# Optimization experiments

Measured on AMD Instinct MI355X. Metric: run time of the kernel, lower is better.

The kernel has to match this reference:

```python
import jax, jax.numpy as jnp
import numpy as np

NEG_SLOPE = 0.2  # PyG GATConv default negative_slope


def _segment_softmax(alpha, dst, n):
    m = jax.ops.segment_max(alpha, dst, num_segments=n)
    m = jnp.where(jnp.isfinite(m), m, 0.0)
    ex = jnp.exp(alpha - m[dst])
    den = jax.ops.segment_sum(ex, dst, num_segments=n)
    return ex / (den[dst] + 1e-16)


def _gat_layer(x, src, dst, eattr, W, att_src, att_dst, We, att_e, b, n):
    h = x @ W                                        # [N, C]
    a = (h @ att_src)[src] + (h @ att_dst)[dst] + (eattr @ We) @ att_e  # [E]
    a = jax.nn.leaky_relu(a, NEG_SLOPE)
    coef = _segment_softmax(a, dst, n)               # edge-wise attention
    out = jax.ops.segment_sum(coef[:, None] * h[src], dst, num_segments=n)
    return out + b


def _glorot(key, shape):
    fan_in, fan_out = shape[0], shape[-1]
    s = jnp.sqrt(6.0 / (fan_in + fan_out))
    return jax.random.uniform(key, shape, jnp.float32, -s, s)


def setup_inputs() -> dict:
    N, E, D, ED = 100000, 1600000, 128, 16
    key = jax.random.key(0)
    ks = jax.random.split(key, 32)
    inp = {
        'x': jax.random.normal(ks[0], (N, D), jnp.float32),
        'edge_index': jax.random.randint(ks[1], (2, E), 0, N, jnp.int64),
        'edge_attr': jax.random.normal(ks[2], (E, ED), jnp.float32),
    }
    dims = [(D, 64), (64, 32), (32, 16)]
    i = 3
    for li, (din, dout) in enumerate(dims, 1):
        inp[f'W{li}'] = _glorot(ks[i], (din, dout)); i += 1
        inp[f'att_src{li}'] = _glorot(ks[i], (dout,)); i += 1
        inp[f'att_dst{li}'] = _glorot(ks[i], (dout,)); i += 1
        inp[f'We{li}'] = _glorot(ks[i], (ED, dout)); i += 1
        inp[f'att_e{li}'] = _glorot(ks[i], (dout,)); i += 1
        inp[f'b{li}'] = jnp.zeros((dout,), jnp.float32)
    return inp


def reference(x, edge_index, edge_attr,
              W1, att_src1, att_dst1, We1, att_e1, b1,
              W2, att_src2, att_dst2, We2, att_e2, b2,
              W3, att_src3, att_dst3, We3, att_e3, b3):
    n = x.shape[0]
    src, dst = edge_index[0], edge_index[1]
    # add self-loops; self-loop edge_attr = mean of incoming edge attrs (fill_value='mean')
    cnt = jax.ops.segment_sum(jnp.ones_like(dst, dtype=edge_attr.dtype), dst, num_segments=n)
    loop_attr = jax.ops.segment_sum(edge_attr, dst, num_segments=n) / jnp.maximum(cnt, 1.0)[:, None]
    loops = jnp.arange(n, dtype=src.dtype)
    src2 = jnp.concatenate([src, loops])
    dst2 = jnp.concatenate([dst, loops])
    ea2 = jnp.concatenate([edge_attr, loop_attr], axis=0)

    h = jax.nn.elu(_gat_layer(x, src2, dst2, ea2, W1, att_src1, att_dst1, We1, att_e1, b1, n))
    h = jax.nn.elu(_gat_layer(h, src2, dst2, ea2, W2, att_src2, att_dst2, We2, att_e2, b2, n))
    z = _gat_layer(h, src2, dst2, ea2, W3, att_src3, att_dst3, We3, att_e3, b3, n)
    return z
```

## Files before the change

### kernel.cpp

```cpp
#include <hip/hip_runtime.h>
#include <hip/hip_bf16.h>

typedef __hip_bfloat16 bf16;

__device__ __forceinline__ float lrelu(float a) { return a > 0.f ? a : 0.2f * a; }
__device__ __forceinline__ int clampi(int v, int hi) { return v < 0 ? 0 : (v >= hi ? hi - 1 : v); }
__device__ __forceinline__ float ldx(const void* p, size_t i, int f32) {
  return f32 ? ((const float*)p)[i] : (float)((const bf16*)p)[i];
}
__device__ __forceinline__ float4 ldx4(const void* p, size_t i, int f32) {
  if (f32) return *(const float4*)((const float*)p + i);
  const __hip_bfloat162* q = (const __hip_bfloat162*)((const bf16*)p + i);
  float2 a = __bfloat1622float2(q[0]), b = __bfloat1622float2(q[1]);
  return make_float4(a.x, a.y, b.x, b.y);
}

__global__ __launch_bounds__(256) void detect_k(const int* __restrict__ ei32,
                                                const unsigned short* __restrict__ xw, int E,
                                                int* __restrict__ flags) {
  __shared__ int s64, sf;
  int t = threadIdx.x;
  if (t == 0) { s64 = 1; sf = 0; }
  __syncthreads();
  int lim = E < 2048 ? E : 2048;
  for (int k = t; k < lim; k += 256)
    if (ei32[2 * k + 1] != 0) atomicAnd(&s64, 0);
  int hit = 0;
  for (int k = t; k < 4096; k += 256) {
    int ex = (xw[k] >> 7) & 0xFF;
    if (ex >= 0xC3) hit = 1;
  }
  if (hit) atomicOr(&sf, 1);
  __syncthreads();
  if (t == 0) { flags[0] = s64; flags[1] = sf; }
}

__global__ __launch_bounds__(256) void count_k(const int* __restrict__ ei32, int E, int N,
                                               const int* __restrict__ flags,
                                               int* __restrict__ cnt) {
  int e = blockIdx.x * blockDim.x + threadIdx.x;
  if (e >= E) return;
  int is64 = flags[0] != 0;
  int d = is64 ? ei32[2 * ((size_t)E + e)] : ei32[(size_t)E + e];
  atomicAdd(&cnt[clampi(d, N)], 1);
}

__global__ __launch_bounds__(1024) void scan1_k(const int* __restrict__ cnt, int* __restrict__ excl,
                                                int* __restrict__ bsum, int n) {
  __shared__ int sh[1024];
  int i = blockIdx.x * 1024 + threadIdx.x;
  int v = (i < n) ? cnt[i] : 0;
  sh[threadIdx.x] = v;
  __syncthreads();
  for (int off = 1; off < 1024; off <<= 1) {
    int t = (threadIdx.x >= off) ? sh[threadIdx.x - off] : 0;
    __syncthreads();
    sh[threadIdx.x] += t;
    __syncthreads();
  }
  if (i < n) excl[i] = sh[threadIdx.x] - v;
  if (threadIdx.x == 1023) bsum[blockIdx.x] = sh[1023];
}

__global__ __launch_bounds__(128) void scan2_k(int* bsum, int nb) {
  __shared__ int sh[128];
  int t = threadIdx.x;
  int v = (t < nb) ? bsum[t] : 0;
  sh[t] = v;
  __syncthreads();
  for (int off = 1; off < 128; off <<= 1) {
    int x = (t >= off) ? sh[t - off] : 0;
    __syncthreads();
    sh[t] += x;
    __syncthreads();
  }
  if (t < nb) bsum[t] = sh[t] - v;
}

__global__ __launch_bounds__(256) void scan3_k(int* __restrict__ row_ptr,
                                               const int* __restrict__ bsum,
                                               int* __restrict__ cur, int n, int E) {
  int i = blockIdx.x * blockDim.x + threadIdx.x;
  if (i < n) {
    int r = row_ptr[i] + bsum[i >> 10];
    row_ptr[i] = r;
    cur[i] = r;
  }
  if (i == 0) row_ptr[n] = E;
}

__global__ __launch_bounds__(64) void wvec_k(const void* We1, const void* ae1, const void* We2,
                                             const void* ae2, const void* We3, const void* ae3,
                                             const int* __restrict__ flags, float* wv) {
  int t = threadIdx.x;
  if (t >= 48) return;
  int f32 = flags[1];
  int l = t >> 4, j = t & 15;
  const void* We = l == 0 ? We1 : (l == 1 ? We2 : We3);
  const void* ae = l == 0 ? ae1 : (l == 1 ? ae2 : ae3);
  int C = l == 0 ? 64 : (l == 1 ? 32 : 16);
  float s = 0.f;
  for (int c = 0; c < C; ++c) s += ldx(We, (size_t)j * C + c, f32) * ldx(ae, c, f32);
  wv[l * 16 + j] = s;
}

__global__ __launch_bounds__(256) void scatter_k(const int* __restrict__ ei32, const void* eattr,
                                                 const float* __restrict__ wv,
                                                 const int* __restrict__ flags,
                                                 int* __restrict__ cur,
                                                 float4* __restrict__ recs, int E, int N) {
  __shared__ float w[48];
  if (threadIdx.x < 48) w[threadIdx.x] = wv[threadIdx.x];
  __syncthreads();
  int e = blockIdx.x * 256 + threadIdx.x;
  if (e >= E) return;
  int is64 = flags[0] != 0, f32 = flags[1] != 0;
  int s = is64 ? ei32[2 * (size_t)e] : ei32[e];
  int d = is64 ? ei32[2 * ((size_t)E + e)] : ei32[(size_t)E + e];
  s = clampi(s, N);
  d = clampi(d, N);
  float v[16];
  if (f32) {
    const float4* p = (const float4*)((const float*)eattr + (size_t)e * 16);
#pragma unroll
    for (int j = 0; j < 4; ++j) {
      float4 t = p[j];
      v[4 * j] = t.x; v[4 * j + 1] = t.y; v[4 * j + 2] = t.z; v[4 * j + 3] = t.w;
    }
  } else {
    const __hip_bfloat162* p = (const __hip_bfloat162*)((const bf16*)eattr + (size_t)e * 16);
#pragma unroll
    for (int j = 0; j < 8; ++j) {
      float2 t = __bfloat1622float2(p[j]);
      v[2 * j] = t.x; v[2 * j + 1] = t.y;
    }
  }
  float q1 = 0.f, q2 = 0.f, q3 = 0.f;
#pragma unroll
  for (int j = 0; j < 16; ++j) {
    q1 += v[j] * w[j];
    q2 += v[j] * w[16 + j];
    q3 += v[j] * w[32 + j];
  }
  int pos = clampi(atomicAdd(&cur[d], 1), E);
  recs[pos] = make_float4(__int_as_float(s), q1, q2, q3);
}

template <int K, int C, bool XEXT>
__global__ __launch_bounds__(256, 4) void mm3_k(const void* Xv, const void* Wv, const void* ats_v,
                                                const void* atd_v, const int* __restrict__ flags,
                                                int N, float* __restrict__ h,
                                                float* __restrict__ as_, float* __restrict__ ad_) {
  static_assert(K == 2 * C, "");
  constexpr int NCG = C / 8;
  constexpr int TM = 512 / NCG;
  __shared__ __align__(16) float Wl[K * C];
  __shared__ __align__(16) float Xl[32 * TM];
  const int f32 = flags[1];
  const int tid = threadIdx.x;
  for (int i = tid; i < K * C; i += 256) Wl[i] = ldx(Wv, i, f32);
  const int cg = tid & (NCG - 1);
  const int ng = tid / NCG;
  const int c0 = cg * 8;
  float ats[8], atd[8];
#pragma unroll
  for (int j = 0; j < 8; ++j) {
    ats[j] = ldx(ats_v, c0 + j, f32);
    atd[j] = ldx(atd_v, c0 + j, f32);
  }
  const int n_base = blockIdx.x * TM;
  float acc[2][8];
#pragma unroll
  for (int i = 0; i < 2; ++i)
#pragma unroll
    for (int j = 0; j < 8; ++j) acc[i][j] = 0.f;

#pragma unroll 1
  for (int kc = 0; kc < K / 32; ++kc) {
    __syncthreads();
#pragma unroll
    for (int t = 0; t < TM / 32; ++t) {
      int f = tid + t * 256;
      int node = f >> 3, kq = f & 7;
      int gn = n_base + node;
      if (gn >= N) gn = N - 1;
      float4 v;
      if (XEXT)
        v = ldx4(Xv, (size_t)gn * K + kc * 32 + kq * 4, f32);
      else
        v = *(const float4*)((const float*)Xv + (size_t)gn * K + kc * 32 + kq * 4);
      int col = node ^ (kq * 4);
      Xl[(kq * 4 + 0) * TM + col] = v.x;
      Xl[(kq * 4 + 1) * TM + col] = v.y;
      Xl[(kq * 4 + 2) * TM + col] = v.z;
      Xl[(kq * 4 + 3) * TM + col] = v.w;
    }
    __syncthreads();
#pragma unroll 8
    for (int kk = 0; kk < 32; ++kk) {
      const float2 xv = *(const float2*)&Xl[kk * TM + ((2 * ng) ^ ((kk >> 2) * 4))];
      const float4 w0 = *(const float4*)&Wl[(kc * 32 + kk) * C + c0];
      const float4 w1 = *(const float4*)&Wl[(kc * 32 + kk) * C + c0 + 4];
      const float ws[8] = {w0.x, w0.y, w0.z, w0.w, w1.x, w1.y, w1.z, w1.w};
#pragma unroll
      for (int j = 0; j < 8; ++j) {
        acc[0][j] += xv.x * ws[j];
        acc[1][j] += xv.y * ws[j];
      }
    }
  }
#pragma unroll
  for (int i = 0; i < 2; ++i) {
    int n = n_base + ng * 2 + i;
    float vs = 0.f, vd = 0.f;
#pragma unroll
    for (int j = 0; j < 8; ++j) {
      vs += acc[i][j] * ats[j];
      vd += acc[i][j] * atd[j];
    }
#pragma unroll
    for (int off = NCG / 2; off > 0; off >>= 1) {
      vs += __shfl_xor(vs, off, NCG);
      vd += __shfl_xor(vd, off, NCG);
    }
    if (n < N) {
      float* hr = &h[(size_t)n * C + c0];
      *(float4*)hr = make_float4(acc[i][0], acc[i][1], acc[i][2], acc[i][3]);
      *(float4*)(hr + 4) = make_float4(acc[i][4], acc[i][5], acc[i][6], acc[i][7]);
      if (cg == 0) {
        as_[n] = vs;
        ad_[n] = vd;
      }
    }
  }
}

template <int C, int QC, bool ELU, bool LAST>
__global__ __launch_bounds__(256) void agg_k(const int* __restrict__ row_ptr,
                                             const float4* __restrict__ recs,
                                             const float* __restrict__ as_,
                                             const float* __restrict__ ad_,
                                             const float* __restrict__ h, const void* b,
                                             const int* __restrict__ flags, void* out, int N,
                                             int E) {
  const int GR = 256 / C;
  __shared__ int ss[256];
  __shared__ float sp[256];
  int lane = threadIdx.x & (C - 1);
  int grp = threadIdx.x / C;
  int slot0 = grp * C;
  int f32 = flags[1];
  float bc = ldx(b, lane, f32);
  for (int n = blockIdx.x * GR + grp; n < N; n += gridDim.x * GR) {
    int start = row_ptr[n], end = row_ptr[n + 1];
    int deg = end > start ? end - start : 0;
    float qsum = 0.f;
    for (int j = lane; j < deg; j += C) {
      float4 r = recs[start + j];
      qsum += ((const float*)&r)[QC];
    }
#pragma unroll
    for (int off = C / 2; off > 0; off >>= 1) qsum += __shfl_xor(qsum, off, C);
    float qloop = qsum / fmaxf((float)deg, 1.0f);
    float adn = ad_[n];
    float m = lrelu(as_[n] + adn + qloop), den = 1.0f;
    float acc = h[(size_t)n * C + lane];
    for (int base = 0; base < deg; base += C) {
      int cnt = deg - base < C ? deg - base : C;
      int sj = 0;
      float aj = -1e30f;
      if (lane < cnt) {
        float4 r = recs[start + base + lane];
        sj = clampi(__float_as_int(r.x), N);
        aj = lrelu(as_[sj] + adn + ((const float*)&r)[QC]);
      }
      float cm = aj;
#pragma unroll
      for (int off = C / 2; off > 0; off >>= 1) cm = fmaxf(cm, __shfl_xor(cm, off, C));
      float nm = fmaxf(m, cm);
      float sc = __expf(m - nm);
      float pj = (lane < cnt) ? __expf(aj - nm) : 0.f;
      float ps = pj;
#pragma unroll
      for (int off = C / 2; off > 0; off >>= 1) ps += __shfl_xor(ps, off, C);
      den = den * sc + ps;
      m = nm;
      ss[slot0 + lane] = sj;
      sp[slot0 + lane] = pj;
      float accs = 0.f;
#pragma unroll 8
      for (int jj = 0; jj < cnt; ++jj) {
        int s = ss[slot0 + jj];
        float p = sp[slot0 + jj];
        accs += p * h[(size_t)s * C + lane];
      }
      acc = acc * sc + accs;
    }
    float o = acc / (den + 1e-16f) + bc;
    if (ELU) o = o > 0.f ? o : (__expf(o) - 1.0f);
    if (LAST && !f32)
      ((bf16*)out)[(size_t)n * C + lane] = (bf16)o;
    else
      ((float*)out)[(size_t)n * C + lane] = o;
  }
}

extern "C" void kernel_launch(void* const* d_in, const int* in_sizes, int n_in, void* d_out,
                              int out_size, void* d_ws, size_t ws_size, hipStream_t stream) {
  const void* x = d_in[0];
  const int* ei32 = (const int*)d_in[1];
  void* eattr = d_in[2];
  const void *W1 = d_in[3], *s1 = d_in[4], *t1 = d_in[5], *We1 = d_in[6], *ae1 = d_in[7],
             *b1 = d_in[8];
  const void *W2 = d_in[9], *s2 = d_in[10], *t2 = d_in[11], *We2 = d_in[12], *ae2 = d_in[13],
             *b2 = d_in[14];
  const void *W3 = d_in[15], *s3 = d_in[16], *t3 = d_in[17], *We3 = d_in[18], *ae3 = d_in[19],
             *b3 = d_in[20];

  const int N = in_sizes[0] / 128;
  const int E = in_sizes[1] / 2;

  char* p = (char*)d_ws;
  auto alloc = [&](size_t bytes) -> void* {
    void* r = (void*)p;
    p += (bytes + 255) & ~(size_t)255;
    return r;
  };
  int* row_ptr = (int*)alloc((size_t)(N + 1) * 4);
  float4* recs = (float4*)alloc((size_t)E * 16);
  int* cnt = (int*)alloc((size_t)N * 4);
  int* cur = (int*)alloc((size_t)N * 4);
  int* bsum = (int*)alloc(128 * 4);
  float* wv = (float*)alloc(64 * 4);
  int* flags = (int*)alloc(256);
  float* as_ = (float*)alloc((size_t)N * 4);
  float* ad_ = (float*)alloc((size_t)N * 4);
  size_t used = (size_t)(p - (char*)d_ws);
  size_t need = 2 * ((size_t)N * 64 * 4 + 256);
  float *bufH, *bufO;
  if (used + need <= ws_size) {
    bufH = (float*)alloc((size_t)N * 64 * 4);
    bufO = (float*)alloc((size_t)N * 64 * 4);
  } else {
    bufH = (float*)eattr;
    bufO = (float*)eattr + (size_t)N * 64;
  }

  hipMemsetAsync(cnt, 0, (size_t)N * 4, stream);
  detect_k<<<1, 256, 0, stream>>>(ei32, (const unsigned short*)x, E, flags);
  count_k<<<(E + 255) / 256, 256, 0, stream>>>(ei32, E, N, flags, cnt);
  int nb = (N + 1023) / 1024;
  scan1_k<<<nb, 1024, 0, stream>>>(cnt, row_ptr, bsum, N);
  scan2_k<<<1, 128, 0, stream>>>(bsum, nb);
  scan3_k<<<(N + 255) / 256, 256, 0, stream>>>(row_ptr, bsum, cur, N, E);
  wvec_k<<<1, 64, 0, stream>>>(We1, ae1, We2, ae2, We3, ae3, flags, wv);
  scatter_k<<<(E + 255) / 256, 256, 0, stream>>>(ei32, eattr, wv, flags, cur, recs, E, N);

  mm3_k<128, 64, true><<<(N + 63) / 64, 256, 0, stream>>>(x, W1, s1, t1, flags, N, bufH, as_, ad_);
  agg_k<64, 1, true, false><<<(N + 3) / 4, 256, 0, stream>>>(row_ptr, recs, as_, ad_, bufH, b1,
                                                             flags, bufO, N, E);
  mm3_k<64, 32, false><<<(N + 127) / 128, 256, 0, stream>>>(bufO, W2, s2, t2, flags, N, bufH, as_,
                                                            ad_);
  agg_k<32, 2, true, false><<<(N + 7) / 8, 256, 0, stream>>>(row_ptr, recs, as_, ad_, bufH, b2,
                                                             flags, bufO, N, E);
  mm3_k<32, 16, false><<<(N + 255) / 256, 256, 0, stream>>>(bufO, W3, s3, t3, flags, N, bufH, as_,
                                                            ad_);
  agg_k<16, 3, false, true><<<(N + 15) / 16, 256, 0, stream>>>(row_ptr, recs, as_, ad_, bufH, b3,
                                                               flags, d_out, N, E);
}
```

Baseline: 588.6 us.

## Replace global atomic CSR scatter with two-pass bucketed binning and local sort

Edges are binned into 32-node buckets in a staging buffer (reusing the hidden-feature buffers), with the in-degree count fused into the same pass, so the separate count kernel goes away. A per-bucket sort kernel then places records into CSR order using shared-memory atomics and writes contiguously. This aims to cut the scattered global atomics and random 16-byte writes of the old scatter, in exchange for an extra staging write and read and an overflow path for buckets that exceed capacity. Per-bucket counters are padded 64 bytes apart to avoid contention.

```diff
diff --git a/kernel.cpp b/kernel.cpp
--- a/kernel.cpp
+++ b/kernel.cpp
@@ -13,6 +13,33 @@
   const __hip_bfloat162* q = (const __hip_bfloat162*)((const bf16*)p + i);
   float2 a = __bfloat1622float2(q[0]), b = __bfloat1622float2(q[1]);
   return make_float4(a.x, a.y, b.x, b.y);
+}
+
+__device__ __forceinline__ void edge_qs(const void* eattr, size_t e, int f32, const float* w,
+                                        float& q1, float& q2, float& q3) {
+  float v[16];
+  if (f32) {
+    const float4* p = (const float4*)((const float*)eattr + e * 16);
+#pragma unroll
+    for (int j = 0; j < 4; ++j) {
+      float4 t = p[j];
+      v[4 * j] = t.x; v[4 * j + 1] = t.y; v[4 * j + 2] = t.z; v[4 * j + 3] = t.w;
+    }
+  } else {
+    const __hip_bfloat162* p = (const __hip_bfloat162*)((const bf16*)eattr + e * 16);
+#pragma unroll
+    for (int j = 0; j < 8; ++j) {
+      float2 t = __bfloat1622float2(p[j]);
+      v[2 * j] = t.x; v[2 * j + 1] = t.y;
+    }
+  }
+  q1 = 0.f; q2 = 0.f; q3 = 0.f;
+#pragma unroll
+  for (int j = 0; j < 16; ++j) {
+    q1 += v[j] * w[j];
+    q2 += v[j] * w[16 + j];
+    q3 += v[j] * w[32 + j];
+  }
 }
 
 __global__ __launch_bounds__(256) void detect_k(const int* __restrict__ ei32,
@@ -104,6 +131,81 @@
   wv[l * 16 + j] = s;
 }
 
+__global__ __launch_bounds__(256) void bin_k(const int* __restrict__ ei32, const void* eattr,
+                                             const float* __restrict__ wv,
+                                             const int* __restrict__ flags, int* __restrict__ cnt,
+                                             int* __restrict__ bcnt, float4* __restrict__ stage,
+                                             int* __restrict__ ovf, int* __restrict__ ovfc, int E,
+                                             int N, int CAP) {
+  __shared__ float w[48];
+  if (threadIdx.x < 48) w[threadIdx.x] = wv[threadIdx.x];
+  __syncthreads();
+  int e = blockIdx.x * 256 + threadIdx.x;
+  if (e >= E) return;
+  int is64 = flags[0] != 0, f32 = flags[1] != 0;
+  int s = is64 ? ei32[2 * (size_t)e] : ei32[e];
+  int d = is64 ? ei32[2 * ((size_t)E + e)] : ei32[(size_t)E + e];
+  s = clampi(s, N);
+  d = clampi(d, N);
+  atomicAdd(&cnt[d], 1);
+  float q1, q2, q3;
+  edge_qs(eattr, (size_t)e, f32, w, q1, q2, q3);
+  int b = d >> 5;
+  int lpos = atomicAdd(&bcnt[b * 16], 1);
+  if (lpos < CAP) {
+    unsigned u = (unsigned)s | ((unsigned)(d & 31) << 20);
+    stage[(size_t)b * CAP + lpos] = make_float4(__uint_as_float(u), q1, q2, q3);
+  } else {
+    int oi = atomicAdd(ovfc, 1);
+    if (oi < E) ovf[oi] = e;
+  }
+}
+
+__global__ __launch_bounds__(256) void sort_k(const int* __restrict__ row_ptr,
+                                              const int* __restrict__ bcnt,
+                                              const float4* __restrict__ stage,
+                                              const int* __restrict__ ovf,
+                                              const int* __restrict__ ovfc,
+                                              const int* __restrict__ ei32, const void* eattr,
+                                              const float* __restrict__ wv,
+                                              const int* __restrict__ flags,
+                                              float4* __restrict__ recs, int E, int N, int CAP) {
+  __shared__ int hcur[32];
+  int b = blockIdx.x;
+  int tid = threadIdx.x;
+  if (tid < 32) hcur[tid] = 0;
+  __syncthreads();
+  int node0 = b << 5;
+  int nrec = bcnt[b * 16];
+  if (nrec > CAP) nrec = CAP;
+  for (int i = tid; i < nrec; i += 256) {
+    float4 r = stage[(size_t)b * CAP + i];
+    unsigned u = __float_as_uint(r.x);
+    int s = (int)(u & 0xFFFFFu);
+    int drel = (int)(u >> 20);
+    int pos = row_ptr[node0 + drel] + atomicAdd(&hcur[drel], 1);
+    recs[clampi(pos, E)] = make_float4(__int_as_float(s), r.y, r.z, r.w);
+  }
+  int oc = *ovfc;
+  if (oc > 0) {
+    if (oc > E) oc = E;
+    __syncthreads();
+    int is64 = flags[0] != 0, f32 = flags[1] != 0;
+    for (int i = tid; i < oc; i += 256) {
+      int e = ovf[i];
+      int d = is64 ? ei32[2 * ((size_t)E + e)] : ei32[(size_t)E + e];
+      d = clampi(d, N);
+      if ((d >> 5) != b) continue;
+      int s = is64 ? ei32[2 * (size_t)e] : ei32[e];
+      s = clampi(s, N);
+      float q1, q2, q3;
+      edge_qs(eattr, (size_t)e, f32, wv, q1, q2, q3);
+      int pos = row_ptr[d] + atomicAdd(&hcur[d & 31], 1);
+      recs[clampi(pos, E)] = make_float4(__int_as_float(s), q1, q2, q3);
+    }
+  }
+}
+
 __global__ __launch_bounds__(256) void scatter_k(const int* __restrict__ ei32, const void* eattr,
                                                  const float* __restrict__ wv,
                                                  const int* __restrict__ flags,
@@ -119,29 +221,8 @@
   int d = is64 ? ei32[2 * ((size_t)E + e)] : ei32[(size_t)E + e];
   s = clampi(s, N);
   d = clampi(d, N);
-  float v[16];
-  if (f32) {
-    const float4* p = (const float4*)((const float*)eattr + (size_t)e * 16);
-#pragma unroll
-    for (int j = 0; j < 4; ++j) {
-      float4 t = p[j];
-      v[4 * j] = t.x; v[4 * j + 1] = t.y; v[4 * j + 2] = t.z; v[4 * j + 3] = t.w;
-    }
-  } else {
-    const __hip_bfloat162* p = (const __hip_bfloat162*)((const bf16*)eattr + (size_t)e * 16);
-#pragma unroll
-    for (int j = 0; j < 8; ++j) {
-      float2 t = __bfloat1622float2(p[j]);
-      v[2 * j] = t.x; v[2 * j + 1] = t.y;
-    }
-  }
-  float q1 = 0.f, q2 = 0.f, q3 = 0.f;
-#pragma unroll
-  for (int j = 0; j < 16; ++j) {
-    q1 += v[j] * w[j];
-    q2 += v[j] * w[16 + j];
-    q3 += v[j] * w[32 + j];
-  }
+  float q1, q2, q3;
+  edge_qs(eattr, (size_t)e, f32, w, q1, q2, q3);
   int pos = clampi(atomicAdd(&cur[d], 1), E);
   recs[pos] = make_float4(__int_as_float(s), q1, q2, q3);
 }
@@ -319,6 +400,7 @@
 
   const int N = in_sizes[0] / 128;
   const int E = in_sizes[1] / 2;
+  const int B = (N + 31) >> 5;
 
   char* p = (char*)d_ws;
   auto alloc = [&](size_t bytes) -> void* {
@@ -335,26 +417,45 @@
   int* flags = (int*)alloc(256);
   float* as_ = (float*)alloc((size_t)N * 4);
   float* ad_ = (float*)alloc((size_t)N * 4);
+  int* bcnt = (int*)alloc((size_t)B * 16 * 4);
+  int* ovf = (int*)alloc((size_t)E * 4);
+  int* ovfc = (int*)alloc(256);
   size_t used = (size_t)(p - (char*)d_ws);
   size_t need = 2 * ((size_t)N * 64 * 4 + 256);
   float *bufH, *bufO;
-  if (used + need <= ws_size) {
+  bool hasbuf = used + need <= ws_size;
+  if (hasbuf) {
     bufH = (float*)alloc((size_t)N * 64 * 4);
     bufO = (float*)alloc((size_t)N * 64 * 4);
   } else {
     bufH = (float*)eattr;
     bufO = (float*)eattr + (size_t)N * 64;
   }
+  size_t stage_bytes = 2 * ((size_t)N * 64 * 4);
+  int CAP = (int)(stage_bytes / ((size_t)B * 16));
+  bool binned = hasbuf && N <= (1 << 20) && CAP >= 64;
 
   hipMemsetAsync(cnt, 0, (size_t)N * 4, stream);
   detect_k<<<1, 256, 0, stream>>>(ei32, (const unsigned short*)x, E, flags);
-  count_k<<<(E + 255) / 256, 256, 0, stream>>>(ei32, E, N, flags, cnt);
+  wvec_k<<<1, 64, 0, stream>>>(We1, ae1, We2, ae2, We3, ae3, flags, wv);
   int nb = (N + 1023) / 1024;
-  scan1_k<<<nb, 1024, 0, stream>>>(cnt, row_ptr, bsum, N);
-  scan2_k<<<1, 128, 0, stream>>>(bsum, nb);
-  scan3_k<<<(N + 255) / 256, 256, 0, stream>>>(row_ptr, bsum, cur, N, E);
-  wvec_k<<<1, 64, 0, stream>>>(We1, ae1, We2, ae2, We3, ae3, flags, wv);
-  scatter_k<<<(E + 255) / 256, 256, 0, stream>>>(ei32, eattr, wv, flags, cur, recs, E, N);
+  if (binned) {
+    hipMemsetAsync(bcnt, 0, (size_t)B * 16 * 4, stream);
+    hipMemsetAsync(ovfc, 0, 4, stream);
+    bin_k<<<(E + 255) / 256, 256, 0, stream>>>(ei32, eattr, wv, flags, cnt, bcnt, (float4*)bufH,
+                                               ovf, ovfc, E, N, CAP);
+    scan1_k<<<nb, 1024, 0, stream>>>(cnt, row_ptr, bsum, N);
+    scan2_k<<<1, 128, 0, stream>>>(bsum, nb);
+    scan3_k<<<(N + 255) / 256, 256, 0, stream>>>(row_ptr, bsum, cur, N, E);
+    sort_k<<<B, 256, 0, stream>>>(row_ptr, bcnt, (const float4*)bufH, ovf, ovfc, ei32, eattr, wv,
+                                  flags, recs, E, N, CAP);
+  } else {
+    count_k<<<(E + 255) / 256, 256, 0, stream>>>(ei32, E, N, flags, cnt);
+    scan1_k<<<nb, 1024, 0, stream>>>(cnt, row_ptr, bsum, N);
+    scan2_k<<<1, 128, 0, stream>>>(bsum, nb);
+    scan3_k<<<(N + 255) / 256, 256, 0, stream>>>(row_ptr, bsum, cur, N, E);
+    scatter_k<<<(E + 255) / 256, 256, 0, stream>>>(ei32, eattr, wv, flags, cur, recs, E, N);
+  }
 
   mm3_k<128, 64, true><<<(N + 63) / 64, 256, 0, stream>>>(x, W1, s1, t1, flags, N, bufH, as_, ad_);
   agg_k<64, 1, true, false><<<(N + 3) / 4, 256, 0, stream>>>(row_ptr, recs, as_, ad_, bufH, b1,
```

After: 598.3 us. No clear change (+1.7%).

## Fuse edge scatter into first-layer matmul launch and fold scan passes

Applied to the files above, without the earlier changes.

Merges the edge-record scatter kernel with the first-layer matmul into one launch, where extra blocks beyond the matmul grid handle 1024 edges each with four edges per thread. It also folds the block-sum scan into scan3 when there are at most 128 blocks, and makes count_k process four edges per thread. The intent is to cut launch overhead and let the memory-bound scatter run alongside the compute-heavy matmul. The fused kernel carries the matmul's shared-memory footprint into the scatter blocks, and every scan3 block redundantly rescans the block sums.

```diff
diff --git a/kernel.cpp b/kernel.cpp
--- a/kernel.cpp
+++ b/kernel.cpp
@@ -13,6 +13,33 @@
   const __hip_bfloat162* q = (const __hip_bfloat162*)((const bf16*)p + i);
   float2 a = __bfloat1622float2(q[0]), b = __bfloat1622float2(q[1]);
   return make_float4(a.x, a.y, b.x, b.y);
+}
+
+__device__ __forceinline__ void edge_qs(const void* eattr, size_t e, int f32, const float* w,
+                                        float& q1, float& q2, float& q3) {
+  float v[16];
+  if (f32) {
+    const float4* p = (const float4*)((const float*)eattr + e * 16);
+#pragma unroll
+    for (int j = 0; j < 4; ++j) {
+      float4 t = p[j];
+      v[4 * j] = t.x; v[4 * j + 1] = t.y; v[4 * j + 2] = t.z; v[4 * j + 3] = t.w;
+    }
+  } else {
+    const __hip_bfloat162* p = (const __hip_bfloat162*)((const bf16*)eattr + e * 16);
+#pragma unroll
+    for (int j = 0; j < 8; ++j) {
+      float2 t = __bfloat1622float2(p[j]);
+      v[2 * j] = t.x; v[2 * j + 1] = t.y;
+    }
+  }
+  q1 = 0.f; q2 = 0.f; q3 = 0.f;
+#pragma unroll
+  for (int j = 0; j < 16; ++j) {
+    q1 += v[j] * w[j];
+    q2 += v[j] * w[16 + j];
+    q3 += v[j] * w[32 + j];
+  }
 }
 
 __global__ __launch_bounds__(256) void detect_k(const int* __restrict__ ei32,
@@ -38,11 +65,16 @@
 __global__ __launch_bounds__(256) void count_k(const int* __restrict__ ei32, int E, int N,
                                                const int* __restrict__ flags,
                                                int* __restrict__ cnt) {
-  int e = blockIdx.x * blockDim.x + threadIdx.x;
-  if (e >= E) return;
   int is64 = flags[0] != 0;
-  int d = is64 ? ei32[2 * ((size_t)E + e)] : ei32[(size_t)E + e];
-  atomicAdd(&cnt[clampi(d, N)], 1);
+  int e0 = blockIdx.x * 1024 + threadIdx.x;
+#pragma unroll
+  for (int i = 0; i < 4; ++i) {
+    int e = e0 + i * 256;
+    if (e < E) {
+      int d = is64 ? ei32[2 * ((size_t)E + e)] : ei32[(size_t)E + e];
+      atomicAdd(&cnt[clampi(d, N)], 1);
+    }
+  }
 }
 
 __global__ __launch_bounds__(1024) void scan1_k(const int* __restrict__ cnt, int* __restrict__ excl,
@@ -77,12 +109,28 @@
   if (t < nb) bsum[t] = sh[t] - v;
 }
 
+template <bool FOLD>
 __global__ __launch_bounds__(256) void scan3_k(int* __restrict__ row_ptr,
                                                const int* __restrict__ bsum,
-                                               int* __restrict__ cur, int n, int E) {
-  int i = blockIdx.x * blockDim.x + threadIdx.x;
+                                               int* __restrict__ cur, int n, int E, int nb) {
+  __shared__ int pref[128];
+  int t = threadIdx.x;
+  if (FOLD) {
+    if (t < 128) pref[t] = (t < nb) ? bsum[t] : 0;
+    __syncthreads();
+    for (int off = 1; off < 128; off <<= 1) {
+      int x = 0;
+      if (t < 128 && t >= off) x = pref[t - off];
+      __syncthreads();
+      if (t < 128) pref[t] += x;
+      __syncthreads();
+    }
+  }
+  int i = blockIdx.x * 256 + t;
   if (i < n) {
-    int r = row_ptr[i] + bsum[i >> 10];
+    int blk = i >> 10;
+    int add = FOLD ? (blk == 0 ? 0 : pref[blk - 1]) : bsum[blk];
+    int r = row_ptr[i] + add;
     row_ptr[i] = r;
     cur[i] = r;
   }
@@ -104,59 +152,14 @@
   wv[l * 16 + j] = s;
 }
 
-__global__ __launch_bounds__(256) void scatter_k(const int* __restrict__ ei32, const void* eattr,
-                                                 const float* __restrict__ wv,
-                                                 const int* __restrict__ flags,
-                                                 int* __restrict__ cur,
-                                                 float4* __restrict__ recs, int E, int N) {
-  __shared__ float w[48];
-  if (threadIdx.x < 48) w[threadIdx.x] = wv[threadIdx.x];
-  __syncthreads();
-  int e = blockIdx.x * 256 + threadIdx.x;
-  if (e >= E) return;
-  int is64 = flags[0] != 0, f32 = flags[1] != 0;
-  int s = is64 ? ei32[2 * (size_t)e] : ei32[e];
-  int d = is64 ? ei32[2 * ((size_t)E + e)] : ei32[(size_t)E + e];
-  s = clampi(s, N);
-  d = clampi(d, N);
-  float v[16];
-  if (f32) {
-    const float4* p = (const float4*)((const float*)eattr + (size_t)e * 16);
-#pragma unroll
-    for (int j = 0; j < 4; ++j) {
-      float4 t = p[j];
-      v[4 * j] = t.x; v[4 * j + 1] = t.y; v[4 * j + 2] = t.z; v[4 * j + 3] = t.w;
-    }
-  } else {
-    const __hip_bfloat162* p = (const __hip_bfloat162*)((const bf16*)eattr + (size_t)e * 16);
-#pragma unroll
-    for (int j = 0; j < 8; ++j) {
-      float2 t = __bfloat1622float2(p[j]);
-      v[2 * j] = t.x; v[2 * j + 1] = t.y;
-    }
-  }
-  float q1 = 0.f, q2 = 0.f, q3 = 0.f;
-#pragma unroll
-  for (int j = 0; j < 16; ++j) {
-    q1 += v[j] * w[j];
-    q2 += v[j] * w[16 + j];
-    q3 += v[j] * w[32 + j];
-  }
-  int pos = clampi(atomicAdd(&cur[d], 1), E);
-  recs[pos] = make_float4(__int_as_float(s), q1, q2, q3);
-}
-
 template <int K, int C, bool XEXT>
-__global__ __launch_bounds__(256, 4) void mm3_k(const void* Xv, const void* Wv, const void* ats_v,
-                                                const void* atd_v, const int* __restrict__ flags,
-                                                int N, float* __restrict__ h,
-                                                float* __restrict__ as_, float* __restrict__ ad_) {
+__device__ __forceinline__ void mm_body(const void* Xv, const void* Wv, const void* ats_v,
+                                        const void* atd_v, int f32, int N, int nblk, float* Wl,
+                                        float* Xl, float* __restrict__ h, float* __restrict__ as_,
+                                        float* __restrict__ ad_) {
   static_assert(K == 2 * C, "");
   constexpr int NCG = C / 8;
   constexpr int TM = 512 / NCG;
-  __shared__ __align__(16) float Wl[K * C];
-  __shared__ __align__(16) float Xl[32 * TM];
-  const int f32 = flags[1];
   const int tid = threadIdx.x;
   for (int i = tid; i < K * C; i += 256) Wl[i] = ldx(Wv, i, f32);
   const int cg = tid & (NCG - 1);
@@ -168,7 +171,7 @@
     ats[j] = ldx(ats_v, c0 + j, f32);
     atd[j] = ldx(atd_v, c0 + j, f32);
   }
-  const int n_base = blockIdx.x * TM;
+  const int n_base = nblk * TM;
   float acc[2][8];
 #pragma unroll
   for (int i = 0; i < 2; ++i)
@@ -233,6 +236,66 @@
       }
     }
   }
+}
+
+template <int K, int C, bool XEXT>
+__global__ __launch_bounds__(256, 4) void mm3_k(const void* Xv, const void* Wv, const void* ats_v,
+                                                const void* atd_v, const int* __restrict__ flags,
+                                                int N, float* __restrict__ h,
+                                                float* __restrict__ as_, float* __restrict__ ad_) {
+  constexpr int TM = 512 / (C / 8);
+  __shared__ __align__(16) float Wl[K * C];
+  __shared__ __align__(16) float Xl[32 * TM];
+  mm_body<K, C, XEXT>(Xv, Wv, ats_v, atd_v, flags[1], N, blockIdx.x, Wl, Xl, h, as_, ad_);
+}
+
+template <int K, int C>
+__global__ __launch_bounds__(256, 4) void mmscat_k(const void* Xv, const void* Wv,
+                                                   const void* ats_v, const void* atd_v,
+                                                   const int* __restrict__ flags, int N,
+                                                   float* __restrict__ h, float* __restrict__ as_,
+                                                   float* __restrict__ ad_, int MMG,
+                                                   const int* __restrict__ ei32, const void* eattr,
+                                                   const float* __restrict__ wv,
+                                                   int* __restrict__ cur,
+                                                   float4* __restrict__ recs, int E) {
+  constexpr int TM = 512 / (C / 8);
+  __shared__ __align__(16) float Wl[K * C];
+  __shared__ __align__(16) float Xl[32 * TM];
+  if ((int)blockIdx.x >= MMG) {
+    if (threadIdx.x < 48) Wl[threadIdx.x] = wv[threadIdx.x];
+    __syncthreads();
+    int chunk = blockIdx.x - MMG;
+    int is64 = flags[0] != 0, f32 = flags[1] != 0;
+    int e0 = chunk * 1024 + threadIdx.x;
+    int ss[4], dd[4], valid[4];
+    float q1[4], q2[4], q3[4];
+#pragma unroll
+    for (int i = 0; i < 4; ++i) {
+      int e = e0 + i * 256;
+      valid[i] = e < E;
+      ss[i] = 0; dd[i] = 0;
+      if (valid[i]) {
+        int s = is64 ? ei32[2 * (size_t)e] : ei32[e];
+        int d = is64 ? ei32[2 * ((size_t)E + e)] : ei32[(size_t)E + e];
+        ss[i] = clampi(s, N);
+        dd[i] = clampi(d, N);
+      }
+    }
+#pragma unroll
+    for (int i = 0; i < 4; ++i)
+      if (valid[i]) edge_qs(eattr, (size_t)(e0 + i * 256), f32, Wl, q1[i], q2[i], q3[i]);
+    int pos[4];
+#pragma unroll
+    for (int i = 0; i < 4; ++i)
+      if (valid[i]) pos[i] = atomicAdd(&cur[dd[i]], 1);
+#pragma unroll
+    for (int i = 0; i < 4; ++i)
+      if (valid[i])
+        recs[clampi(pos[i], E)] = make_float4(__int_as_float(ss[i]), q1[i], q2[i], q3[i]);
+    return;
+  }
+  mm_body<K, C, true>(Xv, Wv, ats_v, atd_v, flags[1], N, blockIdx.x, Wl, Xl, h, as_, ad_);
 }
 
 template <int C, int QC, bool ELU, bool LAST>
@@ -348,15 +411,21 @@
 
   hipMemsetAsync(cnt, 0, (size_t)N * 4, stream);
   detect_k<<<1, 256, 0, stream>>>(ei32, (const unsigned short*)x, E, flags);
-  count_k<<<(E + 255) / 256, 256, 0, stream>>>(ei32, E, N, flags, cnt);
+  wvec_k<<<1, 64, 0, stream>>>(We1, ae1, We2, ae2, We3, ae3, flags, wv);
+  count_k<<<(E + 1023) / 1024, 256, 0, stream>>>(ei32, E, N, flags, cnt);
   int nb = (N + 1023) / 1024;
   scan1_k<<<nb, 1024, 0, stream>>>(cnt, row_ptr, bsum, N);
-  scan2_k<<<1, 128, 0, stream>>>(bsum, nb);
-  scan3_k<<<(N + 255) / 256, 256, 0, stream>>>(row_ptr, bsum, cur, N, E);
-  wvec_k<<<1, 64, 0, stream>>>(We1, ae1, We2, ae2, We3, ae3, flags, wv);
-  scatter_k<<<(E + 255) / 256, 256, 0, stream>>>(ei32, eattr, wv, flags, cur, recs, E, N);
-
-  mm3_k<128, 64, true><<<(N + 63) / 64, 256, 0, stream>>>(x, W1, s1, t1, flags, N, bufH, as_, ad_);
+  if (nb <= 128) {
+    scan3_k<true><<<(N + 255) / 256, 256, 0, stream>>>(row_ptr, bsum, cur, N, E, nb);
+  } else {
+    scan2_k<<<1, 128, 0, stream>>>(bsum, nb);
+    scan3_k<false><<<(N + 255) / 256, 256, 0, stream>>>(row_ptr, bsum, cur, N, E, nb);
+  }
+
+  int MMG = (N + 63) / 64;
+  int SCG = (E + 1023) / 1024;
+  mmscat_k<128, 64><<<MMG + SCG, 256, 0, stream>>>(x, W1, s1, t1, flags, N, bufH, as_, ad_, MMG,
+                                                   ei32, eattr, wv, cur, recs, E);
   agg_k<64, 1, true, false><<<(N + 3) / 4, 256, 0, stream>>>(row_ptr, recs, as_, ad_, bufH, b1,
                                                              flags, bufO, N, E);
   mm3_k<64, 32, false><<<(N + 127) / 128, 256, 0, stream>>>(bufO, W2, s2, t2, flags, N, bufH, as_,
```

After: 595.7 us. Within noise of the previous version (+1.2%).
